# Kernel optimization log

Hardware: AMD Instinct MI355X
Metric: run time of the kernel (lower is better)

The kernel has to match this reference:

```python
import jax, jax.numpy as jnp
import numpy as np
from jax import lax


def _causal_depthwise_conv(x, conv_w, conv_b):
    # x: [B, L, D]; conv_w: [D, 1, K]; conv_b: [D]
    K = conv_w.shape[-1]
    xc = jnp.transpose(x, (0, 2, 1))                      # [B, D, L]
    xc = jnp.pad(xc, ((0, 0), (0, 0), (K - 1, 0)))        # left (causal) pad
    D = xc.shape[1]
    y = lax.conv_general_dilated(
        xc, conv_w, window_strides=(1,), padding='VALID',
        dimension_numbers=('NCH', 'OIH', 'NCH'), feature_group_count=D)
    y = y + conv_b[None, :, None]
    return jnp.transpose(y, (0, 2, 1))                    # [B, L, D]


def setup_inputs() -> dict:
    key = jax.random.key(0)
    ks = jax.random.split(key, 7)
    B, L, Dm, S, K = 4, 4096, 2048, 512, 4
    s = 0.02
    x = jax.random.normal(ks[0], (B, L, Dm), dtype=jnp.float32)
    Wxproj = jax.random.normal(ks[1], (2 * S + 1, Dm), dtype=jnp.float32) * s
    Winproj = jax.random.normal(ks[2], (S, Dm), dtype=jnp.float32) * s
    Woutproj = jax.random.normal(ks[3], (Dm, S), dtype=jnp.float32) * s
    conv_w = jax.random.normal(ks[4], (Dm, 1, K), dtype=jnp.float32) * 0.5
    conv_b = jax.random.normal(ks[5], (Dm,), dtype=jnp.float32) * 0.02
    A_log = jnp.log(jnp.arange(1, S + 1, dtype=jnp.float32))
    D = jnp.ones((Dm,), dtype=jnp.float32)
    return {"x": x, "Wxproj": Wxproj, "Winproj": Winproj, "Woutproj": Woutproj,
            "conv_w": conv_w, "conv_b": conv_b, "A_log": A_log, "D": D}


def reference(x, Wxproj, Winproj, Woutproj, conv_w, conv_b, A_log, D):
    S = A_log.shape[0]
    # causal depthwise conv (Conv1d with padding=K-1, truncated to seq_len)
    x_conv = _causal_depthwise_conv(x, conv_w, conv_b)     # [B, L, Dm]
    # SSM parameters from raw x (matches original: x_proj applied to x, not x_conv)
    ssm_params = jnp.einsum('bld,pd->blp', x, Wxproj)      # [B, L, 2S+1]
    Bmat = ssm_params[..., :S]
    Cmat = ssm_params[..., S:2 * S]
    delta = jax.nn.softplus(ssm_params[..., 2 * S:])       # [B, L, 1]
    A = -jnp.exp(A_log)                                    # [S]
    deltaA = jnp.exp(A[None, None, :] * delta)             # [B, L, S]
    x_state = jnp.einsum('bld,sd->bls', x_conv, Winproj)   # [B, L, S]
    Bu = delta * Bmat * x_state                            # [B, L, S]
    # h_t = deltaA_t * h_{t-1} + Bu_t  via associative scan
    def combine(c1, c2):
        a1, b1 = c1
        a2, b2 = c2
        return a1 * a2, a2 * b1 + b2
    _, h = lax.associative_scan(combine, (deltaA, Bu), axis=1)  # [B, L, S]
    h_mod = Cmat * h
    out = jnp.einsum('bls,ds->bld', h_mod, Woutproj) + D[None, None, :] * x_conv
    return out
```

## Files before the change

### kernel.cpp

```cpp
#include <hip/hip_runtime.h>
#include <math.h>

typedef __bf16 bf16_t;
typedef __bf16 bf16x8 __attribute__((ext_vector_type(8)));
typedef __bf16 bf16x4 __attribute__((ext_vector_type(4)));
typedef float  f32x4  __attribute__((ext_vector_type(4)));
typedef float  f32x16 __attribute__((ext_vector_type(16)));

constexpr int Bb  = 4;
constexpr int L   = 4096;
constexpr int Dm  = 2048;
constexpr int S   = 512;
constexpr int M   = Bb * L;
constexpr int NP  = 2 * S + 1;
constexpr int PST = 1024;
constexpr int CL  = 128;
constexpr int NCH = L / CL;
constexpr int TL  = 32;
constexpr int NTC = L / TL;

#define AS1 __attribute__((address_space(1)))
#define AS3 __attribute__((address_space(3)))

__global__ __launch_bounds__(256)
void f2b_kernel(const float* __restrict__ in, bf16_t* __restrict__ out,
                long out8, long in_elems)
{
    long i = (long)blockIdx.x * 256 + threadIdx.x;
    if (i >= out8) return;
    long e = i * 8;
    bf16x8 o;
    if (e + 8 <= in_elems) {
        float4 v0 = *(const float4*)(in + e);
        float4 v1 = *(const float4*)(in + e + 4);
        o[0] = (bf16_t)v0.x; o[1] = (bf16_t)v0.y;
        o[2] = (bf16_t)v0.z; o[3] = (bf16_t)v0.w;
        o[4] = (bf16_t)v1.x; o[5] = (bf16_t)v1.y;
        o[6] = (bf16_t)v1.z; o[7] = (bf16_t)v1.w;
    } else {
        #pragma unroll
        for (int k = 0; k < 8; ++k)
            o[k] = (e + k < in_elems) ? (bf16_t)in[e + k] : (bf16_t)0.f;
    }
    *(bf16x8*)(out + e) = o;
}

__global__ __launch_bounds__(256)
void conv_fused_kernel(const float* __restrict__ x, const float* __restrict__ w,
                       const float* __restrict__ bias,
                       bf16_t* __restrict__ xcb, bf16_t* __restrict__ xb)
{
    const float4* x4 = (const float4*)x;
    int g   = blockIdx.x * 256 + threadIdx.x;
    int d4  = g & 511;
    int rest = g >> 9;
    int c   = rest & (NTC - 1);
    int b   = rest >> 7;
    int d   = d4 * 4;

    float w0[4], w1[4], w2[4], w3[4];
    *(float4*)w0 = *(const float4*)&w[(d + 0) * 4];
    *(float4*)w1 = *(const float4*)&w[(d + 1) * 4];
    *(float4*)w2 = *(const float4*)&w[(d + 2) * 4];
    *(float4*)w3 = *(const float4*)&w[(d + 3) * 4];
    float4 bs = *(const float4*)&bias[d];

    const int l0 = c * TL;
    const size_t rowbase = (size_t)b * L;

    float4 win[3];
    #pragma unroll
    for (int i = 0; i < 3; ++i) {
        int lp = l0 - 3 + i;
        win[i] = (lp >= 0) ? x4[(rowbase + lp) * 512 + d4]
                           : make_float4(0.f, 0.f, 0.f, 0.f);
    }

    #pragma unroll
    for (int t = 0; t < TL; ++t) {
        size_t ri = (rowbase + l0 + t) * 512 + d4;
        float4 cur = x4[ri];
        float4 acc = bs;
        acc.x = fmaf(win[0].x, w0[0], acc.x);
        acc.y = fmaf(win[0].y, w1[0], acc.y);
        acc.z = fmaf(win[0].z, w2[0], acc.z);
        acc.w = fmaf(win[0].w, w3[0], acc.w);
        acc.x = fmaf(win[1].x, w0[1], acc.x);
        acc.y = fmaf(win[1].y, w1[1], acc.y);
        acc.z = fmaf(win[1].z, w2[1], acc.z);
        acc.w = fmaf(win[1].w, w3[1], acc.w);
        acc.x = fmaf(win[2].x, w0[2], acc.x);
        acc.y = fmaf(win[2].y, w1[2], acc.y);
        acc.z = fmaf(win[2].z, w2[2], acc.z);
        acc.w = fmaf(win[2].w, w3[2], acc.w);
        acc.x = fmaf(cur.x, w0[3], acc.x);
        acc.y = fmaf(cur.y, w1[3], acc.y);
        acc.z = fmaf(cur.z, w2[3], acc.z);
        acc.w = fmaf(cur.w, w3[3], acc.w);

        bf16x4 oc, ox;
        oc[0] = (bf16_t)acc.x; oc[1] = (bf16_t)acc.y;
        oc[2] = (bf16_t)acc.z; oc[3] = (bf16_t)acc.w;
        ox[0] = (bf16_t)cur.x; ox[1] = (bf16_t)cur.y;
        ox[2] = (bf16_t)cur.z; ox[3] = (bf16_t)cur.w;
        *(bf16x4*)(xcb + ri * 4) = oc;
        *(bf16x4*)(xb  + ri * 4) = ox;

        win[0] = win[1]; win[1] = win[2]; win[2] = cur;
    }
}

__global__ __launch_bounds__(256)
void gemv_delta(const bf16_t* __restrict__ x_bf, const bf16_t* __restrict__ wdt,
                float* __restrict__ delta)
{
    int m    = blockIdx.x * 4 + (threadIdx.x >> 6);
    int lane = threadIdx.x & 63;
    const bf16x8* xr = (const bf16x8*)(x_bf + (size_t)m * Dm);
    const bf16x8* wr = (const bf16x8*)wdt;
    float s = 0.f;
    #pragma unroll
    for (int i = 0; i < 4; ++i) {
        bf16x8 a = xr[i * 64 + lane];
        bf16x8 b = wr[i * 64 + lane];
        #pragma unroll
        for (int j = 0; j < 8; ++j) s += (float)a[j] * (float)b[j];
    }
    #pragma unroll
    for (int off = 32; off >= 1; off >>= 1) s += __shfl_xor(s, off, 64);
    if (lane == 0) {
        delta[m] = (s > 20.f) ? s : log1pf(__expf(s));
    }
}

__device__ __forceinline__ void stage_slabA(const bf16_t* __restrict__ A,
    bf16_t* lds, int ldsbase, int row0, int K, int kcol, int mh,
    int wid, int lrow, int cswz)
{
    #pragma unroll
    for (int round = 0; round < 2; ++round) {
        int Rb = round * 128 + mh * 64 + wid * 8;
        const bf16_t* src = A + (size_t)(row0 + Rb + lrow) * K + kcol + cswz;
        __builtin_amdgcn_global_load_lds(
            (AS1 void*)src, (AS3 void*)(lds + ldsbase + Rb * 64), 16, 0, 0);
    }
}

__device__ __forceinline__ void stage_slabB(const bf16_t* __restrict__ B,
    bf16_t* lds, int ldsbase, int col0, int K, int kcol, int nh,
    int wid, int lrow, int cswz)
{
    #pragma unroll
    for (int round = 0; round < 2; ++round) {
        int c  = round * 8 + wid;
        int Rb = (c >> 2) * 64 + nh * 32 + (c & 3) * 8;
        const bf16_t* src = B + (size_t)(col0 + Rb + lrow) * K + kcol + cswz;
        __builtin_amdgcn_global_load_lds(
            (AS1 void*)src, (AS3 void*)(lds + ldsbase + Rb * 64), 16, 0, 0);
    }
}

template <int MH>
__device__ __forceinline__ void load_fragsA32(const bf16_t* lds, int Abase,
    int wm, int l31, int kh, bf16x8 (&af)[2][4])
{
    #pragma unroll
    for (int mi2 = 0; mi2 < 2; ++mi2) {
        const int R = wm * 128 + (MH * 2 + mi2) * 32 + l31;
        #pragma unroll
        for (int ks = 0; ks < 4; ++ks)
            af[mi2][ks] = *(const bf16x8*)(lds + Abase + R * 64 +
                            ((ks * 16 + kh * 8) ^ ((R & 7) << 3)));
    }
}

template <int NH>
__device__ __forceinline__ void load_fragsB32(const bf16_t* lds, int Bbase,
    int wn, int l31, int kh, bf16x8 (&bfr)[4])
{
    const int R = wn * 64 + NH * 32 + l31;
    #pragma unroll
    for (int ks = 0; ks < 4; ++ks)
        bfr[ks] = *(const bf16x8*)(lds + Bbase + R * 64 +
                    ((ks * 16 + kh * 8) ^ ((R & 7) << 3)));
}

template <int MH, int NH>
__device__ __forceinline__ void do_mfma32(bf16x8 (&af)[2][4], bf16x8 (&bfr)[4],
                                          f32x16 (&acc)[4][2])
{
    __builtin_amdgcn_s_setprio(1);
    #pragma unroll
    for (int ks = 0; ks < 4; ++ks)
        #pragma unroll
        for (int mi2 = 0; mi2 < 2; ++mi2)
            acc[MH * 2 + mi2][NH] = __builtin_amdgcn_mfma_f32_32x32x16_bf16(
                af[mi2][ks], bfr[ks], acc[MH * 2 + mi2][NH], 0, 0, 0);
    __builtin_amdgcn_s_setprio(0);
}

#define WAITBAR() do { \
    asm volatile("s_waitcnt vmcnt(4)" ::: "memory"); \
    __builtin_amdgcn_s_barrier(); } while (0)

template <int EPI>
__global__ __launch_bounds__(512, 2)
void gemm8p(const bf16_t* __restrict__ A, const bf16_t* __restrict__ B,
            int N, int K, int NT,
            bf16_t* __restrict__ Cb, float* __restrict__ Cf,
            const float* __restrict__ e0, const bf16_t* __restrict__ eb)
{
    extern __shared__ __align__(16) char smem_raw[];
    bf16_t* lds = (bf16_t*)smem_raw;

    const int tid  = threadIdx.x;
    const int lane = tid & 63;
    const int wid  = tid >> 6;
    const int wm   = wid >> 2;
    const int wn   = wid & 3;
    const int l31  = lane & 31;
    const int kh   = lane >> 5;
    const int row0 = blockIdx.x * 256;
    const int col0 = blockIdx.y * 256;
    const int lrow = lane >> 3;
    const int cswz = 8 * ((lane & 7) ^ lrow);

    f32x16 acc[4][2];
    #pragma unroll
    for (int i = 0; i < 4; ++i)
        #pragma unroll
        for (int j = 0; j < 2; ++j)
            #pragma unroll
            for (int g = 0; g < 16; ++g) acc[i][j][g] = 0.f;

    stage_slabA(A, lds, 0,     row0, K, 0, 0, wid, lrow, cswz);
    stage_slabB(B, lds, 16384, col0, K, 0, 0, wid, lrow, cswz);
    stage_slabB(B, lds, 16384, col0, K, 0, 1, wid, lrow, cswz);
    stage_slabA(A, lds, 0,     row0, K, 0, 1, wid, lrow, cswz);

    for (int kt = 0; kt < NT; ++kt) {
        const int cur = kt & 1, nxt = cur ^ 1;
        const int Abase = cur * 32768, Bbase = cur * 32768 + 16384;
        const int An = nxt * 32768,   Bn = nxt * 32768 + 16384;
        const int kc = (kt + 1 < NT ? kt + 1 : kt) * 64;

        bf16x8 af[2][4], bfr[4];

        WAITBAR();
        load_fragsA32<0>(lds, Abase, wm, l31, kh, af);
        load_fragsB32<0>(lds, Bbase, wn, l31, kh, bfr);
        stage_slabA(A, lds, An, row0, K, kc, 0, wid, lrow, cswz);
        do_mfma32<0, 0>(af, bfr, acc);

        WAITBAR();
        load_fragsB32<1>(lds, Bbase, wn, l31, kh, bfr);
        stage_slabB(B, lds, Bn, col0, K, kc, 0, wid, lrow, cswz);
        do_mfma32<0, 1>(af, bfr, acc);

        WAITBAR();
        load_fragsA32<1>(lds, Abase, wm, l31, kh, af);
        stage_slabB(B, lds, Bn, col0, K, kc, 1, wid, lrow, cswz);
        do_mfma32<1, 1>(af, bfr, acc);

        load_fragsB32<0>(lds, Bbase, wn, l31, kh, bfr);
        stage_slabA(A, lds, An, row0, K, kc, 1, wid, lrow, cswz);
        do_mfma32<1, 0>(af, bfr, acc);
    }

    #pragma unroll
    for (int mi = 0; mi < 4; ++mi) {
        #pragma unroll
        for (int nj = 0; nj < 2; ++nj) {
            #pragma unroll
            for (int rg = 0; rg < 16; ++rg) {
                int mr = row0 + wm * 128 + mi * 32 + (rg & 3) + 8 * (rg >> 2) + 4 * kh;
                int nc = col0 + wn * 64 + nj * 32 + l31;
                float v = acc[mi][nj][rg];
                if (EPI == 0) {
                    Cb[(size_t)mr * PST + nc] = (bf16_t)v;
                } else if (EPI == 1) {
                    float Bm = (float)eb[(size_t)mr * PST + nc];
                    Cf[(size_t)mr * N + nc] = e0[mr] * Bm * v;
                } else {
                    float xc = (float)eb[(size_t)mr * N + nc];
                    Cf[(size_t)mr * N + nc] = v + e0[nc] * xc;
                }
            }
        }
    }
}

__global__ __launch_bounds__(256)
void scan_pass1(const float* __restrict__ Bu, const float* __restrict__ delta,
                const float* __restrict__ A_log,
                float* __restrict__ cP, float* __restrict__ cH)
{
    int s = blockIdx.x * 256 + threadIdx.x;
    int c = blockIdx.y;
    int b = blockIdx.z;
    float Acoef = -expf(A_log[s]);
    float P = 1.f, h = 0.f;
    int mbase = b * L + c * CL;
    for (int t = 0; t < CL; ++t) {
        float a = __expf(Acoef * delta[mbase + t]);
        float u = Bu[(size_t)(mbase + t) * S + s];
        h = fmaf(a, h, u);
        P *= a;
    }
    int id = b * S + s;
    cP[(size_t)id * NCH + c] = P;
    cH[(size_t)id * NCH + c] = h;
}

__global__ __launch_bounds__(256)
void scan_pass2(const float* __restrict__ cP, const float* __restrict__ cH,
                float* __restrict__ init)
{
    int id = blockIdx.x * 256 + threadIdx.x;
    if (id < Bb * S) {
        float h = 0.f;
        for (int c = 0; c < NCH; ++c) {
            init[(size_t)id * NCH + c] = h;
            h = fmaf(cP[(size_t)id * NCH + c], h, cH[(size_t)id * NCH + c]);
        }
    }
}

__global__ __launch_bounds__(256)
void scan_pass3(const float* __restrict__ Bu, const float* __restrict__ delta,
                const bf16_t* __restrict__ params_bf,
                const float* __restrict__ A_log,
                const float* __restrict__ init, bf16_t* __restrict__ hmod)
{
    int s = blockIdx.x * 256 + threadIdx.x;
    int c = blockIdx.y;
    int b = blockIdx.z;
    float Acoef = -expf(A_log[s]);
    float h = init[(size_t)(b * S + s) * NCH + c];
    int mbase = b * L + c * CL;
    for (int t = 0; t < CL; ++t) {
        int m = mbase + t;
        float a = __expf(Acoef * delta[m]);
        float u = Bu[(size_t)m * S + s];
        h = fmaf(a, h, u);
        float Cm = (float)params_bf[(size_t)m * PST + S + s];
        hmod[(size_t)m * S + s] = (bf16_t)(Cm * h);
    }
}

extern "C" void kernel_launch(void* const* d_in, const int* in_sizes, int n_in,
                              void* d_out, int out_size, void* d_ws, size_t ws_size,
                              hipStream_t stream)
{
    const float* x        = (const float*)d_in[0];
    const float* Wxproj   = (const float*)d_in[1];
    const float* Winproj  = (const float*)d_in[2];
    const float* Woutproj = (const float*)d_in[3];
    const float* conv_w   = (const float*)d_in[4];
    const float* conv_b   = (const float*)d_in[5];
    const float* A_log    = (const float*)d_in[6];
    const float* Dvec     = (const float*)d_in[7];
    float* out = (float*)d_out;

    float* ws_Bu    = (float*)d_ws;
    float* ws_delta = ws_Bu + (size_t)M * S;
    float* ws_cP    = ws_delta + M;
    float* ws_cH    = ws_cP + (size_t)Bb * S * NCH;
    float* ws_init  = ws_cH + (size_t)Bb * S * NCH;
    bf16_t* params_bf = (bf16_t*)(ws_init + (size_t)Bb * S * NCH);
    bf16_t* x_bf      = params_bf + (size_t)M * PST;
    bf16_t* hmod_bf   = x_bf;
    bf16_t* xconv_bf  = x_bf + (size_t)M * Dm;
    bf16_t* Wx_bf     = xconv_bf + (size_t)M * Dm;
    bf16_t* Win_bf    = Wx_bf + (size_t)NP * Dm;
    bf16_t* Wout_bf   = Win_bf + (size_t)S * Dm;

    hipFuncSetAttribute((const void*)gemm8p<0>,
                        hipFuncAttributeMaxDynamicSharedMemorySize, 131072);
    hipFuncSetAttribute((const void*)gemm8p<1>,
                        hipFuncAttributeMaxDynamicSharedMemorySize, 131072);
    hipFuncSetAttribute((const void*)gemm8p<2>,
                        hipFuncAttributeMaxDynamicSharedMemorySize, 131072);

    long wx8 = (long)NP * Dm / 8;
    f2b_kernel<<<(wx8 + 255) / 256, 256, 0, stream>>>(Wxproj, Wx_bf, wx8, (long)NP * Dm);
    long wi8 = (long)S * Dm / 8;
    f2b_kernel<<<(wi8 + 255) / 256, 256, 0, stream>>>(Winproj, Win_bf, wi8, (long)S * Dm);
    f2b_kernel<<<(wi8 + 255) / 256, 256, 0, stream>>>(Woutproj, Wout_bf, wi8, (long)Dm * S);

    conv_fused_kernel<<<(Bb * NTC * 512) / 256, 256, 0, stream>>>(
        x, conv_w, conv_b, xconv_bf, x_bf);

    dim3 g1(M / 256, PST / 256);
    gemm8p<0><<<g1, 512, 131072, stream>>>(x_bf, Wx_bf, PST, Dm, Dm / 64,
                                           params_bf, nullptr, nullptr, nullptr);

    gemv_delta<<<M / 4, 256, 0, stream>>>(x_bf, Wx_bf + (size_t)PST * Dm, ws_delta);

    dim3 g2(M / 256, S / 256);
    gemm8p<1><<<g2, 512, 131072, stream>>>(xconv_bf, Win_bf, S, Dm, Dm / 64,
                                           nullptr, ws_Bu, ws_delta, params_bf);

    dim3 gs(S / 256, NCH, Bb);
    scan_pass1<<<gs, 256, 0, stream>>>(ws_Bu, ws_delta, A_log, ws_cP, ws_cH);
    scan_pass2<<<(Bb * S) / 256, 256, 0, stream>>>(ws_cP, ws_cH, ws_init);
    scan_pass3<<<gs, 256, 0, stream>>>(ws_Bu, ws_delta, params_bf, A_log,
                                       ws_init, hmod_bf);

    dim3 g3(M / 256, Dm / 256);
    gemm8p<2><<<g3, 512, 131072, stream>>>(hmod_bf, Wout_bf, Dm, S, S / 64,
                                           nullptr, out, Dvec, xconv_bf);
}
```

Before: 302.8 us.

## Add 128-row GEMM variant for input projection and widen conv to 8 channels

```diff
diff --git a/kernel.cpp b/kernel.cpp
--- a/kernel.cpp
+++ b/kernel.cpp
@@ -46,67 +46,68 @@
 }
 
 __global__ __launch_bounds__(256)
-void conv_fused_kernel(const float* __restrict__ x, const float* __restrict__ w,
-                       const float* __restrict__ bias,
-                       bf16_t* __restrict__ xcb, bf16_t* __restrict__ xb)
+void conv_fused8(const float* __restrict__ x, const float* __restrict__ w,
+                 const float* __restrict__ bias,
+                 bf16_t* __restrict__ xcb, bf16_t* __restrict__ xb)
 {
     const float4* x4 = (const float4*)x;
-    int g   = blockIdx.x * 256 + threadIdx.x;
-    int d4  = g & 511;
-    int rest = g >> 9;
-    int c   = rest & (NTC - 1);
-    int b   = rest >> 7;
-    int d   = d4 * 4;
-
-    float w0[4], w1[4], w2[4], w3[4];
-    *(float4*)w0 = *(const float4*)&w[(d + 0) * 4];
-    *(float4*)w1 = *(const float4*)&w[(d + 1) * 4];
-    *(float4*)w2 = *(const float4*)&w[(d + 2) * 4];
-    *(float4*)w3 = *(const float4*)&w[(d + 3) * 4];
-    float4 bs = *(const float4*)&bias[d];
+    int g    = blockIdx.x * 256 + threadIdx.x;
+    int d8   = g & 255;
+    int rest = g >> 8;
+    int c    = rest & (NTC - 1);
+    int b    = rest >> 7;
+    int d    = d8 * 8;
+
+    float wv[8][4];
+    #pragma unroll
+    for (int j = 0; j < 8; ++j)
+        *(float4*)wv[j] = *(const float4*)&w[(d + j) * 4];
+    float bsv[8];
+    *(float4*)&bsv[0] = *(const float4*)&bias[d];
+    *(float4*)&bsv[4] = *(const float4*)&bias[d + 4];
 
     const int l0 = c * TL;
     const size_t rowbase = (size_t)b * L;
 
-    float4 win[3];
+    float win[3][8];
     #pragma unroll
     for (int i = 0; i < 3; ++i) {
         int lp = l0 - 3 + i;
-        win[i] = (lp >= 0) ? x4[(rowbase + lp) * 512 + d4]
-                           : make_float4(0.f, 0.f, 0.f, 0.f);
-    }
-
-    #pragma unroll
+        if (lp >= 0) {
+            size_t rb4 = (rowbase + lp) * 512 + d8 * 2;
+            *(float4*)&win[i][0] = x4[rb4];
+            *(float4*)&win[i][4] = x4[rb4 + 1];
+        } else {
+            #pragma unroll
+            for (int j = 0; j < 8; ++j) win[i][j] = 0.f;
+        }
+    }
+
     for (int t = 0; t < TL; ++t) {
-        size_t ri = (rowbase + l0 + t) * 512 + d4;
-        float4 cur = x4[ri];
-        float4 acc = bs;
-        acc.x = fmaf(win[0].x, w0[0], acc.x);
-        acc.y = fmaf(win[0].y, w1[0], acc.y);
-        acc.z = fmaf(win[0].z, w2[0], acc.z);
-        acc.w = fmaf(win[0].w, w3[0], acc.w);
-        acc.x = fmaf(win[1].x, w0[1], acc.x);
-        acc.y = fmaf(win[1].y, w1[1], acc.y);
-        acc.z = fmaf(win[1].z, w2[1], acc.z);
-        acc.w = fmaf(win[1].w, w3[1], acc.w);
-        acc.x = fmaf(win[2].x, w0[2], acc.x);
-        acc.y = fmaf(win[2].y, w1[2], acc.y);
-        acc.z = fmaf(win[2].z, w2[2], acc.z);
-        acc.w = fmaf(win[2].w, w3[2], acc.w);
-        acc.x = fmaf(cur.x, w0[3], acc.x);
-        acc.y = fmaf(cur.y, w1[3], acc.y);
-        acc.z = fmaf(cur.z, w2[3], acc.z);
-        acc.w = fmaf(cur.w, w3[3], acc.w);
-
-        bf16x4 oc, ox;
-        oc[0] = (bf16_t)acc.x; oc[1] = (bf16_t)acc.y;
-        oc[2] = (bf16_t)acc.z; oc[3] = (bf16_t)acc.w;
-        ox[0] = (bf16_t)cur.x; ox[1] = (bf16_t)cur.y;
-        ox[2] = (bf16_t)cur.z; ox[3] = (bf16_t)cur.w;
-        *(bf16x4*)(xcb + ri * 4) = oc;
-        *(bf16x4*)(xb  + ri * 4) = ox;
-
-        win[0] = win[1]; win[1] = win[2]; win[2] = cur;
+        size_t m = rowbase + l0 + t;
+        size_t rb4 = m * 512 + d8 * 2;
+        float cur[8];
+        *(float4*)&cur[0] = x4[rb4];
+        *(float4*)&cur[4] = x4[rb4 + 1];
+
+        bf16x8 oc, ox;
+        #pragma unroll
+        for (int j = 0; j < 8; ++j) {
+            float a = bsv[j];
+            a = fmaf(win[0][j], wv[j][0], a);
+            a = fmaf(win[1][j], wv[j][1], a);
+            a = fmaf(win[2][j], wv[j][2], a);
+            a = fmaf(cur[j],    wv[j][3], a);
+            oc[j] = (bf16_t)a;
+            ox[j] = (bf16_t)cur[j];
+        }
+        *(bf16x8*)(xcb + m * Dm + d) = oc;
+        *(bf16x8*)(xb  + m * Dm + d) = ox;
+
+        #pragma unroll
+        for (int j = 0; j < 8; ++j) {
+            win[0][j] = win[1][j]; win[1][j] = win[2][j]; win[2][j] = cur[j];
+        }
     }
 }
 
@@ -140,6 +141,19 @@
     #pragma unroll
     for (int round = 0; round < 2; ++round) {
         int Rb = round * 128 + mh * 64 + wid * 8;
+        const bf16_t* src = A + (size_t)(row0 + Rb + lrow) * K + kcol + cswz;
+        __builtin_amdgcn_global_load_lds(
+            (AS1 void*)src, (AS3 void*)(lds + ldsbase + Rb * 64), 16, 0, 0);
+    }
+}
+
+__device__ __forceinline__ void stage_slabA128(const bf16_t* __restrict__ A,
+    bf16_t* lds, int ldsbase, int row0, int K, int kcol,
+    int wid, int lrow, int cswz)
+{
+    #pragma unroll
+    for (int round = 0; round < 2; ++round) {
+        int Rb = round * 64 + wid * 8;
         const bf16_t* src = A + (size_t)(row0 + Rb + lrow) * K + kcol + cswz;
         __builtin_amdgcn_global_load_lds(
             (AS1 void*)src, (AS3 void*)(lds + ldsbase + Rb * 64), 16, 0, 0);
@@ -174,6 +188,17 @@
     }
 }
 
+template <int MI>
+__device__ __forceinline__ void load_fragsA32h(const bf16_t* lds, int Abase,
+    int wm, int l31, int kh, bf16x8 (&af)[4])
+{
+    const int R = wm * 64 + MI * 32 + l31;
+    #pragma unroll
+    for (int ks = 0; ks < 4; ++ks)
+        af[ks] = *(const bf16x8*)(lds + Abase + R * 64 +
+                    ((ks * 16 + kh * 8) ^ ((R & 7) << 3)));
+}
+
 template <int NH>
 __device__ __forceinline__ void load_fragsB32(const bf16_t* lds, int Bbase,
     int wn, int l31, int kh, bf16x8 (&bfr)[4])
@@ -199,8 +224,20 @@
     __builtin_amdgcn_s_setprio(0);
 }
 
-#define WAITBAR() do { \
-    asm volatile("s_waitcnt vmcnt(4)" ::: "memory"); \
+template <int MI, int NJ>
+__device__ __forceinline__ void do_mfma32h(bf16x8 (&af)[4], bf16x8 (&bfr)[4],
+                                           f32x16 (&acc)[2][2])
+{
+    __builtin_amdgcn_s_setprio(1);
+    #pragma unroll
+    for (int ks = 0; ks < 4; ++ks)
+        acc[MI][NJ] = __builtin_amdgcn_mfma_f32_32x32x16_bf16(
+            af[ks], bfr[ks], acc[MI][NJ], 0, 0, 0);
+    __builtin_amdgcn_s_setprio(0);
+}
+
+#define WAITBAR(N) do { \
+    asm volatile("s_waitcnt vmcnt(" #N ")" ::: "memory"); \
     __builtin_amdgcn_s_barrier(); } while (0)
 
 template <int EPI>
@@ -246,18 +283,18 @@
 
         bf16x8 af[2][4], bfr[4];
 
-        WAITBAR();
+        WAITBAR(4);
         load_fragsA32<0>(lds, Abase, wm, l31, kh, af);
         load_fragsB32<0>(lds, Bbase, wn, l31, kh, bfr);
         stage_slabA(A, lds, An, row0, K, kc, 0, wid, lrow, cswz);
         do_mfma32<0, 0>(af, bfr, acc);
 
-        WAITBAR();
+        WAITBAR(4);
         load_fragsB32<1>(lds, Bbase, wn, l31, kh, bfr);
         stage_slabB(B, lds, Bn, col0, K, kc, 0, wid, lrow, cswz);
         do_mfma32<0, 1>(af, bfr, acc);
 
-        WAITBAR();
+        WAITBAR(4);
         load_fragsA32<1>(lds, Abase, wm, l31, kh, af);
         stage_slabB(B, lds, Bn, col0, K, kc, 1, wid, lrow, cswz);
         do_mfma32<1, 1>(af, bfr, acc);
@@ -278,13 +315,85 @@
                 float v = acc[mi][nj][rg];
                 if (EPI == 0) {
                     Cb[(size_t)mr * PST + nc] = (bf16_t)v;
-                } else if (EPI == 1) {
-                    float Bm = (float)eb[(size_t)mr * PST + nc];
-                    Cf[(size_t)mr * N + nc] = e0[mr] * Bm * v;
                 } else {
                     float xc = (float)eb[(size_t)mr * N + nc];
                     Cf[(size_t)mr * N + nc] = v + e0[nc] * xc;
                 }
+            }
+        }
+    }
+}
+
+__global__ __launch_bounds__(512, 2)
+void gemm8ph(const bf16_t* __restrict__ A, const bf16_t* __restrict__ B,
+             int N, int K, int NT,
+             float* __restrict__ Cf,
+             const float* __restrict__ e0, const bf16_t* __restrict__ eb)
+{
+    extern __shared__ __align__(16) char smem_raw[];
+    bf16_t* lds = (bf16_t*)smem_raw;
+
+    const int tid  = threadIdx.x;
+    const int lane = tid & 63;
+    const int wid  = tid >> 6;
+    const int wm   = wid >> 2;
+    const int wn   = wid & 3;
+    const int l31  = lane & 31;
+    const int kh   = lane >> 5;
+    const int row0 = blockIdx.x * 128;
+    const int col0 = blockIdx.y * 256;
+    const int lrow = lane >> 3;
+    const int cswz = 8 * ((lane & 7) ^ lrow);
+
+    f32x16 acc[2][2];
+    #pragma unroll
+    for (int i = 0; i < 2; ++i)
+        #pragma unroll
+        for (int j = 0; j < 2; ++j)
+            #pragma unroll
+            for (int g = 0; g < 16; ++g) acc[i][j][g] = 0.f;
+
+    stage_slabA128(A, lds, 0,    row0, K, 0, wid, lrow, cswz);
+    stage_slabB(B, lds, 8192, col0, K, 0, 0, wid, lrow, cswz);
+    stage_slabB(B, lds, 8192, col0, K, 0, 1, wid, lrow, cswz);
+
+    for (int kt = 0; kt < NT; ++kt) {
+        const int cur = kt & 1, nxt = cur ^ 1;
+        const int Abase = cur * 24576, Bbase = cur * 24576 + 8192;
+        const int An = nxt * 24576,   Bn = nxt * 24576 + 8192;
+        const int kc = (kt + 1 < NT ? kt + 1 : kt) * 64;
+
+        bf16x8 af[4], bfr[4];
+
+        WAITBAR(2);
+        load_fragsA32h<0>(lds, Abase, wm, l31, kh, af);
+        load_fragsB32<0>(lds, Bbase, wn, l31, kh, bfr);
+        stage_slabA128(A, lds, An, row0, K, kc, wid, lrow, cswz);
+        do_mfma32h<0, 0>(af, bfr, acc);
+
+        WAITBAR(2);
+        load_fragsB32<1>(lds, Bbase, wn, l31, kh, bfr);
+        stage_slabB(B, lds, Bn, col0, K, kc, 0, wid, lrow, cswz);
+        do_mfma32h<0, 1>(af, bfr, acc);
+
+        load_fragsA32h<1>(lds, Abase, wm, l31, kh, af);
+        stage_slabB(B, lds, Bn, col0, K, kc, 1, wid, lrow, cswz);
+        do_mfma32h<1, 1>(af, bfr, acc);
+
+        load_fragsB32<0>(lds, Bbase, wn, l31, kh, bfr);
+        do_mfma32h<1, 0>(af, bfr, acc);
+    }
+
+    #pragma unroll
+    for (int mi = 0; mi < 2; ++mi) {
+        #pragma unroll
+        for (int nj = 0; nj < 2; ++nj) {
+            #pragma unroll
+            for (int rg = 0; rg < 16; ++rg) {
+                int mr = row0 + wm * 64 + mi * 32 + (rg & 3) + 8 * (rg >> 2) + 4 * kh;
+                int nc = col0 + wn * 64 + nj * 32 + l31;
+                float Bm = (float)eb[(size_t)mr * PST + nc];
+                Cf[(size_t)mr * N + nc] = e0[mr] * Bm * acc[mi][nj][rg];
             }
         }
     }
@@ -377,10 +486,10 @@
 
     hipFuncSetAttribute((const void*)gemm8p<0>,
                         hipFuncAttributeMaxDynamicSharedMemorySize, 131072);
-    hipFuncSetAttribute((const void*)gemm8p<1>,
-                        hipFuncAttributeMaxDynamicSharedMemorySize, 131072);
     hipFuncSetAttribute((const void*)gemm8p<2>,
                         hipFuncAttributeMaxDynamicSharedMemorySize, 131072);
+    hipFuncSetAttribute((const void*)gemm8ph,
+                        hipFuncAttributeMaxDynamicSharedMemorySize, 98304);
 
     long wx8 = (long)NP * Dm / 8;
     f2b_kernel<<<(wx8 + 255) / 256, 256, 0, stream>>>(Wxproj, Wx_bf, wx8, (long)NP * Dm);
@@ -388,7 +497,7 @@
     f2b_kernel<<<(wi8 + 255) / 256, 256, 0, stream>>>(Winproj, Win_bf, wi8, (long)S * Dm);
     f2b_kernel<<<(wi8 + 255) / 256, 256, 0, stream>>>(Woutproj, Wout_bf, wi8, (long)Dm * S);
 
-    conv_fused_kernel<<<(Bb * NTC * 512) / 256, 256, 0, stream>>>(
+    conv_fused8<<<(Bb * NTC * 256) / 256, 256, 0, stream>>>(
         x, conv_w, conv_b, xconv_bf, x_bf);
 
     dim3 g1(M / 256, PST / 256);
@@ -397,9 +506,9 @@
 
     gemv_delta<<<M / 4, 256, 0, stream>>>(x_bf, Wx_bf + (size_t)PST * Dm, ws_delta);
 
-    dim3 g2(M / 256, S / 256);
-    gemm8p<1><<<g2, 512, 131072, stream>>>(xconv_bf, Win_bf, S, Dm, Dm / 64,
-                                           nullptr, ws_Bu, ws_delta, params_bf);
+    dim3 g2(M / 128, S / 256);
+    gemm8ph<<<g2, 512, 98304, stream>>>(xconv_bf, Win_bf, S, Dm, Dm / 64,
+                                        ws_Bu, ws_delta, params_bf);
 
     dim3 gs(S / 256, NCH, Bb);
     scan_pass1<<<gs, 256, 0, stream>>>(ws_Bu, ws_delta, A_log, ws_cP, ws_cH);
```

Result: faster. 293.5 us (-3.1%).
